# Performance work log

Hardware: AMD Instinct MI355X
Metric: run time of the kernel (lower is better)

Reference implementation:

```python
import math
import jax, jax.numpy as jnp
import numpy as np

B, T, C = 4, 2048, 1024
NH, HD = 16, 64  # n_head, head_dim
RANK = 128


def setup_inputs() -> dict:
    key = jax.random.key(0)
    ks = jax.random.split(key, 9)
    s_in = 1.0 / math.sqrt(C)
    s_r = 1.0 / math.sqrt(RANK)
    inp = {"x": jax.random.normal(ks[0], (B, T, C), dtype=jnp.float32)}
    for i, name in enumerate(["q", "k", "v", "c"]):
        inp[name + "A"] = jax.random.normal(ks[1 + 2 * i], (RANK, C), dtype=jnp.float32) * s_in
        inp[name + "B"] = jax.random.normal(ks[2 + 2 * i], (C, RANK), dtype=jnp.float32) * s_r
    return inp


def _lowrank(x, A, Bf):
    # HarmonicLinear: rank-r factorized linear, W = Bf @ A, y = x @ W^T
    return (x @ A.T) @ Bf.T


def reference(x, qA, qB, kA, kB, vA, vB, cA, cB):
    b, t, c = x.shape
    q = _lowrank(x, qA, qB).reshape(b, t, NH, HD).transpose(0, 2, 1, 3)  # [b,h,t,d]
    k = _lowrank(x, kA, kB).reshape(b, t, NH, HD).transpose(0, 2, 1, 3)
    v = _lowrank(x, vA, vB).reshape(b, t, NH, HD).transpose(0, 2, 1, 3)
    att = jnp.einsum("bhqd,bhkd->bhqk", q, k) * (1.0 / math.sqrt(HD))
    causal = jnp.tril(jnp.ones((t, t), dtype=bool))
    att = jnp.where(causal, att, -jnp.inf)
    att = jax.nn.softmax(att, axis=-1)
    y = jnp.einsum("bhqk,bhkd->bhqd", att, v)
    y = y.transpose(0, 2, 1, 3).reshape(b, t, c)
    return _lowrank(y, cA, cB)
```

## Files before the change

### kernel.cpp

```cpp
#include <hip/hip_runtime.h>

typedef unsigned short u16;
typedef __attribute__((ext_vector_type(8))) short bf16x8;
typedef __attribute__((ext_vector_type(4))) float f32x4;
typedef __attribute__((ext_vector_type(16))) float f32x16;
typedef __attribute__((ext_vector_type(4))) int i32x4;

typedef const __attribute__((address_space(1))) void gvoid_t;
typedef __attribute__((address_space(3))) void svoid_t;

__device__ __forceinline__ u16 f2bf(float f) {
  unsigned u = __builtin_bit_cast(unsigned, f);
  u += 0x7fffu + ((u >> 16) & 1u);
  return (u16)(u >> 16);
}

__device__ __forceinline__ unsigned cvtpk(float a, float b) {
  unsigned r;
  asm("v_cvt_pk_bf16_f32 %0, %1, %2" : "=v"(r) : "v"(a), "v"(b));
  return r;
}

__device__ __forceinline__ void gload_lds16(const u16* g, u16* ldsbase) {
  __builtin_amdgcn_global_load_lds((gvoid_t*)g, (svoid_t*)ldsbase, 16, 0, 0);
}

__device__ __forceinline__ void mfma16(f32x4& d, bf16x8 a, bf16x8 b) {
  asm("v_mfma_f32_16x16x32_bf16 %0, %1, %2, %0" : "+v"(d) : "v"(a), "v"(b));
}
__device__ __forceinline__ void mfma32(f32x16& d, bf16x8 a, bf16x8 b) {
  asm("v_mfma_f32_32x32x16_bf16 %0, %1, %2, %0" : "+v"(d) : "v"(a), "v"(b));
}
__device__ __forceinline__ void mfma_fence4(f32x4& a, f32x4& b, f32x4& c, f32x4& d) {
  asm volatile("s_nop 7\n\ts_nop 7" : "+v"(a), "+v"(b), "+v"(c), "+v"(d));
}
__device__ __forceinline__ void fence16x2(f32x16& a, f32x16& b) {
  asm volatile("s_nop 7\n\ts_nop 7\n\ts_nop 7" : "+v"(a), "+v"(b));
}

struct W8 { const float* s[8]; };
__global__ __launch_bounds__(256) void cvt_w_kernel(W8 w, u16* __restrict__ wb) {
  const int b = blockIdx.x;
  const int wi = b >> 7;
  const int wo = b & 127;
  const float* src = w.s[wi];
  u16* dst = wb + (size_t)wi * 131072;
  int i = (wo * 256 + (int)threadIdx.x) * 4;
  float4 v = *(const float4*)(src + i);
  ushort4 o = {f2bf(v.x), f2bf(v.y), f2bf(v.z), f2bf(v.w)};
  *(ushort4*)(dst + i) = o;
}

struct G3 { const u16* A[3]; const u16* B[3]; void* C[3]; float osc[3]; int vt[3]; };

template <typename OutT, int BM, bool CVTA, bool XCDMAP>
__global__ __launch_bounds__(256) void gemm_nt(G3 g, int M, int N, int K) {
  constexpr int NI = (BM == 128) ? 4 : 2;
  __shared__ __align__(16) u16 At[2][BM * 64];
  __shared__ __align__(16) u16 Bt[2][128 * 64];
  int bx = blockIdx.x, by = blockIdx.y, bz = blockIdx.z;
  if constexpr (XCDMAP) {
    const int xcd = bx & 7, slot = bx >> 3;
    bz = slot % 3;
    bx = xcd * 16 + slot / 3;
    by = 0;
  }
  const int z = bz;
  const u16* __restrict__ A = g.A[z];
  const float* __restrict__ Af = (const float*)g.A[z];
  const u16* __restrict__ Bw = g.B[z];
  const float osc = g.osc[z];
  const int tid = threadIdx.x;
  const int lane = tid & 63, w = tid >> 6;
  const int wm = (BM == 128) ? (w >> 1) : 0;
  const int wn = (BM == 128) ? (w & 1) : w;
  constexpr int WNW = (BM == 128) ? 64 : 32;
  const int l15 = lane & 15, l4 = lane >> 4;
  const int row0 = bx * BM, col0 = by * 128;
  const int srow = lane >> 3;
  const int schunk = ((lane & 7) ^ srow) * 8;
  const u16* Ag = A + (size_t)(row0 + w * 8 + srow) * K + schunk;
  const u16* Bg = Bw + (size_t)(col0 + w * 8 + srow) * K + schunk;
  f32x4 acc[4][NI] = {};
  float4 ax[4];
  auto STAGEB = [&](int k0, int buf) {
#pragma unroll
    for (int i = 0; i < 4; ++i)
      gload_lds16(Bg + (size_t)i * 32 * K + k0, &Bt[buf][(w * 8 + i * 32) * 64]);
  };
  auto STAGEA_G = [&](int k0, int buf) {
#pragma unroll
    for (int i = 0; i < BM / 32; ++i)
      gload_lds16(Ag + (size_t)i * 32 * K + k0, &At[buf][(w * 8 + i * 32) * 64]);
  };
  auto LOADA = [&](int k0) {
#pragma unroll
    for (int i = 0; i < BM / 32; ++i) {
      const float* src = Af + (size_t)(row0 + w * 8 + i * 32 + srow) * K + k0 + schunk;
      ax[2 * i] = *(const float4*)src;
      ax[2 * i + 1] = *(const float4*)(src + 4);
    }
  };
  auto WRITEA = [&](int buf) {
#pragma unroll
    for (int i = 0; i < BM / 32; ++i) {
      i32x4 d;
      d[0] = (int)cvtpk(ax[2 * i].x, ax[2 * i].y);
      d[1] = (int)cvtpk(ax[2 * i].z, ax[2 * i].w);
      d[2] = (int)cvtpk(ax[2 * i + 1].x, ax[2 * i + 1].y);
      d[3] = (int)cvtpk(ax[2 * i + 1].z, ax[2 * i + 1].w);
      *(i32x4*)&At[buf][(w * 8 + i * 32 + srow) * 64 + (lane & 7) * 8] = d;
    }
  };
  if constexpr (CVTA) LOADA(0); else STAGEA_G(0, 0);
  STAGEB(0, 0);
  if constexpr (CVTA) WRITEA(0);
  asm volatile("s_waitcnt vmcnt(0)" ::: "memory");
  __syncthreads();
  const int nk = K >> 6;
  for (int t = 0; t < nk; ++t) {
    const int cur = t & 1;
    if (t + 1 < nk) {
      if constexpr (CVTA) LOADA((t + 1) << 6); else STAGEA_G((t + 1) << 6, cur ^ 1);
      STAGEB((t + 1) << 6, cur ^ 1);
    }
#pragma unroll
    for (int kk = 0; kk < 64; kk += 32) {
      bf16x8 af[4], bfr[NI];
#pragma unroll
      for (int mi = 0; mi < 4; ++mi) {
        const int r = wm * 64 + mi * 16 + l15;
        af[mi] = *(const bf16x8*)&At[cur][r * 64 + ((kk + 8 * l4) ^ ((r & 7) << 3))];
      }
#pragma unroll
      for (int ni = 0; ni < NI; ++ni) {
        const int r = wn * WNW + ni * 16 + l15;
        bfr[ni] = *(const bf16x8*)&Bt[cur][r * 64 + ((kk + 8 * l4) ^ ((r & 7) << 3))];
      }
#pragma unroll
      for (int mi = 0; mi < 4; ++mi)
#pragma unroll
        for (int ni = 0; ni < NI; ++ni) mfma16(acc[mi][ni], af[mi], bfr[ni]);
    }
    if constexpr (CVTA) { if (t + 1 < nk) WRITEA(cur ^ 1); }
    asm volatile("s_waitcnt vmcnt(0)" ::: "memory");
    __syncthreads();
  }
#pragma unroll
  for (int mi = 0; mi < 4; ++mi)
    mfma_fence4(acc[mi][0], acc[mi][NI - 1], acc[mi][0], acc[mi][NI - 1]);
  if (g.vt[z]) {
    u16* VTo = (u16*)g.C[z];
    const int bbv = row0 >> 11;
#pragma unroll
    for (int mi = 0; mi < 4; ++mi) {
      const int r = row0 + wm * 64 + mi * 16 + l4 * 4;
      const int t0 = r & 2047;
#pragma unroll
      for (int ni = 0; ni < NI; ++ni) {
        const int c = col0 + wn * WNW + ni * 16 + l15;
        ushort4 ov = {f2bf(acc[mi][ni][0] * osc), f2bf(acc[mi][ni][1] * osc),
                      f2bf(acc[mi][ni][2] * osc), f2bf(acc[mi][ni][3] * osc)};
        *(ushort4*)(VTo + ((size_t)(bbv * 1024 + c)) * 2048 + t0) = ov;
      }
    }
  } else {
    OutT* __restrict__ C = (OutT*)g.C[z];
#pragma unroll
    for (int mi = 0; mi < 4; ++mi) {
      const int r = row0 + wm * 64 + mi * 16 + l4 * 4;
#pragma unroll
      for (int ni = 0; ni < NI; ++ni) {
        const int c = col0 + wn * WNW + ni * 16 + l15;
#pragma unroll
        for (int j = 0; j < 4; ++j) {
          float v = acc[mi][ni][j] * osc;
          if constexpr (sizeof(OutT) == 2)
            ((u16*)C)[(size_t)(r + j) * N + c] = f2bf(v);
          else
            ((float*)C)[(size_t)(r + j) * N + c] = v;
        }
      }
    }
  }
}

__global__ __launch_bounds__(256, 4) void attn_kernel(const u16* __restrict__ Qg,
                                                      const u16* __restrict__ Kg,
                                                      const u16* __restrict__ VTg,
                                                      u16* __restrict__ Yg) {
  __shared__ __align__(16) u16 Kt[2][64 * 64];
  __shared__ __align__(16) u16 Vt[2][64 * 64];
  const int tid = threadIdx.x;
  const int lane = tid & 63, w = tid >> 6;
  const int l31 = lane & 31, hi = lane >> 5;
  const int f = blockIdx.x;
  const int s = f >> 6;
  const int qt = (s < 4) ? 15 - 2 * s : (s < 8) ? 2 * s - 8
               : (s < 12) ? 30 - 2 * s : 2 * s - 23;
  const int bhid = f & 63;
  const int bb = bhid >> 4, h = bhid & 15;
  const size_t rb = (size_t)bb * 2048;
  const int h64 = h * 64;
  const int qb0 = qt << 7;
  const int qg = qb0 + w * 32 + l31;
  const int qend = qb0 + w * 32 + 31;
  const u16* Kbh = Kg + rb * 1024 + h64;
  const u16* VTbh = VTg + (size_t)bhid * 64 * 2048;
  const int srow = lane >> 3;
  const int schunk = ((lane & 7) ^ srow) * 8;

  bf16x8 qf[4];
#pragma unroll
  for (int kd = 0; kd < 4; ++kd)
    qf[kd] = *(const bf16x8*)(Qg + (rb + qg) * 1024 + h64 + kd * 16 + 8 * hi);

  f32x16 o0 = {}, o1 = {};
  const float MNEG = -30000.f;
  float lrun = 0.f;

  auto STAGE = [&](int it, int buf) {
    const int kv0 = it << 6;
    const int r0 = w * 16;
#pragma unroll
    for (int i = 0; i < 2; ++i) {
      gload_lds16(Kbh + (size_t)(kv0 + r0 + i * 8 + srow) * 1024 + schunk,
                  &Kt[buf][(r0 + i * 8) * 64]);
      gload_lds16(VTbh + (size_t)(r0 + i * 8 + srow) * 2048 + kv0 + schunk,
                  &Vt[buf][(r0 + i * 8) * 64]);
    }
  };
  STAGE(0, 0);
  asm volatile("s_waitcnt vmcnt(0)" ::: "memory");
  __syncthreads();

  const int nkv = 2 * qt + 2;
  for (int t = 0; t < nkv; ++t) {
    const int cur = t & 1;
    if (t + 1 < nkv) STAGE(t + 1, cur ^ 1);
    const int kv0 = t << 6;
    if (kv0 <= qend) {
      f32x16 s0 = {}, s1 = {};
      __builtin_amdgcn_s_setprio(1);
#pragma unroll
      for (int kd = 0; kd < 4; ++kd) {
        const int col = (kd * 16 + 8 * hi) ^ ((l31 & 7) << 3);
        bf16x8 kf0 = *(const bf16x8*)&Kt[cur][l31 * 64 + col];
        bf16x8 kf1 = *(const bf16x8*)&Kt[cur][(32 + l31) * 64 + col];
        mfma32(s0, kf0, qf[kd]);
        mfma32(s1, kf1, qf[kd]);
      }
      __builtin_amdgcn_s_setprio(0);
      fence16x2(s0, s1);
      if (kv0 + 63 > qb0 + w * 32) {
        const int lim = qg - (kv0 + 4 * hi);
#pragma unroll
        for (int r = 0; r < 16; ++r) {
          const int C0 = (r & 3) + 8 * (r >> 2);
          if (C0 > lim) s0[r] = MNEG;
          if (C0 + 32 > lim) s1[r] = MNEG;
        }
      }
#pragma unroll
      for (int r = 0; r < 16; ++r) {
        s0[r] = __builtin_amdgcn_exp2f(s0[r]);
        s1[r] = __builtin_amdgcn_exp2f(s1[r]);
      }
      float t8[8];
#pragma unroll
      for (int r = 0; r < 8; ++r)
        t8[r] = (s0[2 * r] + s0[2 * r + 1]) + (s1[2 * r] + s1[2 * r + 1]);
      float rs = ((t8[0] + t8[1]) + (t8[2] + t8[3])) +
                 ((t8[4] + t8[5]) + (t8[6] + t8[7]));
      lrun += rs + __shfl_xor(rs, 32, 64);
      i32x4 paw[4];
#pragma unroll
      for (int tl = 0; tl < 2; ++tl) {
        const f32x16& p = tl ? s1 : s0;
#pragma unroll
        for (int ks = 0; ks < 2; ++ks) {
          unsigned pk0 = cvtpk(p[8 * ks + 0], p[8 * ks + 1]);
          unsigned pk1 = cvtpk(p[8 * ks + 2], p[8 * ks + 3]);
          unsigned pk2 = cvtpk(p[8 * ks + 4], p[8 * ks + 5]);
          unsigned pk3 = cvtpk(p[8 * ks + 6], p[8 * ks + 7]);
          asm("v_permlane32_swap_b32 %0, %1" : "+v"(pk0), "+v"(pk2));
          asm("v_permlane32_swap_b32 %0, %1" : "+v"(pk1), "+v"(pk3));
          i32x4 A;
          A[0] = (int)pk0;
          A[1] = (int)pk1;
          A[2] = (int)pk2;
          A[3] = (int)pk3;
          paw[tl * 2 + ks] = A;
        }
      }
      asm volatile("s_nop 1");
      __builtin_amdgcn_s_setprio(1);
#pragma unroll
      for (int tl = 0; tl < 2; ++tl)
#pragma unroll
        for (int ks = 0; ks < 2; ++ks) {
          bf16x8 pa = __builtin_bit_cast(bf16x8, paw[tl * 2 + ks]);
          const int kvc = tl * 32 + ks * 16 + 8 * hi;
#pragma unroll
          for (int dt = 0; dt < 2; ++dt) {
            const int row = dt * 32 + l31;
            bf16x8 vf = *(const bf16x8*)&Vt[cur][row * 64 + (kvc ^ ((l31 & 7) << 3))];
            if (dt == 0) mfma32(o0, vf, pa);
            else         mfma32(o1, vf, pa);
          }
        }
      __builtin_amdgcn_s_setprio(0);
    }
    asm volatile("s_waitcnt vmcnt(0)" ::: "memory");
    __syncthreads();
  }
  fence16x2(o0, o1);
  const float inv = 1.f / lrun;
  u16* Yrow = Yg + (rb + qg) * 1024 + h64;
#pragma unroll
  for (int r = 0; r < 16; r += 2) {
    const int dbase = (r & 3) + 8 * (r >> 2) + 4 * hi;
    *(unsigned*)(Yrow + dbase) = cvtpk(o0[r] * inv, o0[r + 1] * inv);
    *(unsigned*)(Yrow + 32 + dbase) = cvtpk(o1[r] * inv, o1[r + 1] * inv);
  }
}

extern "C" void kernel_launch(void* const* d_in, const int* in_sizes, int n_in,
                              void* d_out, int out_size, void* d_ws, size_t ws_size,
                              hipStream_t stream) {
  const float* x = (const float*)d_in[0];
  char* ws = (char*)d_ws;
  u16* xb = (u16*)ws;
  u16* wb = (u16*)(ws + (16u << 20));
  u16* Rq = (u16*)(ws + (18u << 20));
  u16* Rk = (u16*)(ws + (20u << 20));
  u16* Rv = (u16*)(ws + (22u << 20));
  u16* Ry = (u16*)(ws + (24u << 20));
  u16* Qb = (u16*)(ws + (26u << 20));
  u16* Kb = (u16*)(ws + (42u << 20));
  u16* VT = (u16*)(ws + (58u << 20));
  const int WSZ = 131072;
  const float SC = 0.18033688011112042f;

  W8 wp;
  for (int i = 0; i < 8; ++i) wp.s[i] = (const float*)d_in[1 + i];
  cvt_w_kernel<<<1024, 256, 0, stream>>>(wp, wb);

  G3 g1;
  g1.A[0] = g1.A[1] = g1.A[2] = (const u16*)x;
  g1.B[0] = wb; g1.B[1] = wb + 2 * WSZ; g1.B[2] = wb + 4 * WSZ;
  g1.C[0] = Rq; g1.C[1] = Rk; g1.C[2] = Rv;
  g1.osc[0] = g1.osc[1] = g1.osc[2] = 1.f;
  g1.vt[0] = g1.vt[1] = g1.vt[2] = 0;
  gemm_nt<u16, 64, true, true><<<dim3(384), 256, 0, stream>>>(g1, 8192, 128, 1024);

  G3 g2;
  g2.A[0] = Rq; g2.A[1] = Rk; g2.A[2] = Rv;
  g2.B[0] = wb + 1 * WSZ; g2.B[1] = wb + 3 * WSZ; g2.B[2] = wb + 5 * WSZ;
  g2.C[0] = Qb; g2.C[1] = Kb; g2.C[2] = VT;
  g2.osc[0] = SC; g2.osc[1] = 1.f; g2.osc[2] = 1.f;
  g2.vt[0] = 0; g2.vt[1] = 0; g2.vt[2] = 1;
  gemm_nt<u16, 128, false, false><<<dim3(64, 8, 3), 256, 0, stream>>>(g2, 8192, 1024, 128);

  attn_kernel<<<dim3(1024), 256, 0, stream>>>(Qb, Kb, VT, xb);

  G3 g3;
  g3.A[0] = g3.A[1] = g3.A[2] = xb;
  g3.B[0] = g3.B[1] = g3.B[2] = wb + 6 * WSZ;
  g3.C[0] = g3.C[1] = g3.C[2] = Ry;
  g3.osc[0] = g3.osc[1] = g3.osc[2] = 1.f;
  g3.vt[0] = g3.vt[1] = g3.vt[2] = 0;
  gemm_nt<u16, 64, false, false><<<dim3(128, 1, 1), 256, 0, stream>>>(g3, 8192, 128, 1024);
  G3 g4;
  g4.A[0] = g4.A[1] = g4.A[2] = Ry;
  g4.B[0] = g4.B[1] = g4.B[2] = wb + 7 * WSZ;
  g4.C[0] = g4.C[1] = g4.C[2] = d_out;
  g4.osc[0] = g4.osc[1] = g4.osc[2] = 1.f;
  g4.vt[0] = g4.vt[1] = g4.vt[2] = 0;
  gemm_nt<float, 128, false, false><<<dim3(64, 8, 1), 256, 0, stream>>>(g4, 8192, 1024, 128);
}
```

Baseline: 122.9 us.

## Split-K the rank-reduction GEMMs and shrink tiles for more parallelism

The first low-rank projection GEMM now uses 32-row tiles, launching twice as many blocks. The output projection's first GEMM is split along K into two halves, each writing fp32 partials. The second GEMM sums those partials while converting to bf16 and uses 64-row tiles. The aim is to fill more CUs on the narrow N=128 GEMMs, which launched too few blocks. In exchange it adds fp32 partial traffic, an extra read, and smaller tiles with less reuse.

```diff
diff --git a/kernel.cpp b/kernel.cpp
--- a/kernel.cpp
+++ b/kernel.cpp
@@ -31,8 +31,8 @@
 __device__ __forceinline__ void mfma32(f32x16& d, bf16x8 a, bf16x8 b) {
   asm("v_mfma_f32_32x32x16_bf16 %0, %1, %2, %0" : "+v"(d) : "v"(a), "v"(b));
 }
-__device__ __forceinline__ void mfma_fence4(f32x4& a, f32x4& b, f32x4& c, f32x4& d) {
-  asm volatile("s_nop 7\n\ts_nop 7" : "+v"(a), "+v"(b), "+v"(c), "+v"(d));
+__device__ __forceinline__ void mfma_fence2(f32x4& a, f32x4& b) {
+  asm volatile("s_nop 7\n\ts_nop 7" : "+v"(a), "+v"(b));
 }
 __device__ __forceinline__ void fence16x2(f32x16& a, f32x16& b) {
   asm volatile("s_nop 7\n\ts_nop 7\n\ts_nop 7" : "+v"(a), "+v"(b));
@@ -51,25 +51,32 @@
   *(ushort4*)(dst + i) = o;
 }
 
-struct G3 { const u16* A[3]; const u16* B[3]; void* C[3]; float osc[3]; int vt[3]; };
-
-template <typename OutT, int BM, bool CVTA, bool XCDMAP>
+struct G3 {
+  const u16* A[3]; const float* A2[3]; const u16* B[3]; void* C[3];
+  float osc[3]; int vt[3]; int koff[3]; int klen;
+};
+
+template <typename OutT, int BM, int CVTMODE, bool XCDMAP>
 __global__ __launch_bounds__(256) void gemm_nt(G3 g, int M, int N, int K) {
+  constexpr int MI = (BM == 32) ? 2 : 4;
   constexpr int NI = (BM == 128) ? 4 : 2;
   __shared__ __align__(16) u16 At[2][BM * 64];
   __shared__ __align__(16) u16 Bt[2][128 * 64];
   int bx = blockIdx.x, by = blockIdx.y, bz = blockIdx.z;
   if constexpr (XCDMAP) {
+    const int rpx = (M / BM) >> 3;
     const int xcd = bx & 7, slot = bx >> 3;
     bz = slot % 3;
-    bx = xcd * 16 + slot / 3;
+    bx = xcd * rpx + slot / 3;
     by = 0;
   }
   const int z = bz;
   const u16* __restrict__ A = g.A[z];
   const float* __restrict__ Af = (const float*)g.A[z];
+  const float* __restrict__ Af2 = g.A2[z];
   const u16* __restrict__ Bw = g.B[z];
   const float osc = g.osc[z];
+  const int koff = g.koff[z];
   const int tid = threadIdx.x;
   const int lane = tid & 63, w = tid >> 6;
   const int wm = (BM == 128) ? (w >> 1) : 0;
@@ -81,8 +88,8 @@
   const int schunk = ((lane & 7) ^ srow) * 8;
   const u16* Ag = A + (size_t)(row0 + w * 8 + srow) * K + schunk;
   const u16* Bg = Bw + (size_t)(col0 + w * 8 + srow) * K + schunk;
-  f32x4 acc[4][NI] = {};
-  float4 ax[4];
+  f32x4 acc[MI][NI] = {};
+  float4 ax[2 * (BM / 32)], ax2[CVTMODE == 2 ? 2 * (BM / 32) : 1];
   auto STAGEB = [&](int k0, int buf) {
 #pragma unroll
     for (int i = 0; i < 4; ++i)
@@ -96,39 +103,50 @@
   auto LOADA = [&](int k0) {
 #pragma unroll
     for (int i = 0; i < BM / 32; ++i) {
-      const float* src = Af + (size_t)(row0 + w * 8 + i * 32 + srow) * K + k0 + schunk;
-      ax[2 * i] = *(const float4*)src;
-      ax[2 * i + 1] = *(const float4*)(src + 4);
+      const size_t off = (size_t)(row0 + w * 8 + i * 32 + srow) * K + k0 + schunk;
+      ax[2 * i] = *(const float4*)(Af + off);
+      ax[2 * i + 1] = *(const float4*)(Af + off + 4);
+      if constexpr (CVTMODE == 2) {
+        ax2[2 * i] = *(const float4*)(Af2 + off);
+        ax2[2 * i + 1] = *(const float4*)(Af2 + off + 4);
+      }
     }
   };
   auto WRITEA = [&](int buf) {
 #pragma unroll
     for (int i = 0; i < BM / 32; ++i) {
+      float4 a0 = ax[2 * i], a1 = ax[2 * i + 1];
+      if constexpr (CVTMODE == 2) {
+        const float4 b0 = ax2[2 * i], b1 = ax2[2 * i + 1];
+        a0.x += b0.x; a0.y += b0.y; a0.z += b0.z; a0.w += b0.w;
+        a1.x += b1.x; a1.y += b1.y; a1.z += b1.z; a1.w += b1.w;
+      }
       i32x4 d;
-      d[0] = (int)cvtpk(ax[2 * i].x, ax[2 * i].y);
-      d[1] = (int)cvtpk(ax[2 * i].z, ax[2 * i].w);
-      d[2] = (int)cvtpk(ax[2 * i + 1].x, ax[2 * i + 1].y);
-      d[3] = (int)cvtpk(ax[2 * i + 1].z, ax[2 * i + 1].w);
+      d[0] = (int)cvtpk(a0.x, a0.y);
+      d[1] = (int)cvtpk(a0.z, a0.w);
+      d[2] = (int)cvtpk(a1.x, a1.y);
+      d[3] = (int)cvtpk(a1.z, a1.w);
       *(i32x4*)&At[buf][(w * 8 + i * 32 + srow) * 64 + (lane & 7) * 8] = d;
     }
   };
-  if constexpr (CVTA) LOADA(0); else STAGEA_G(0, 0);
-  STAGEB(0, 0);
-  if constexpr (CVTA) WRITEA(0);
+  if constexpr (CVTMODE) LOADA(koff); else STAGEA_G(koff, 0);
+  STAGEB(koff, 0);
+  if constexpr (CVTMODE) WRITEA(0);
   asm volatile("s_waitcnt vmcnt(0)" ::: "memory");
   __syncthreads();
-  const int nk = K >> 6;
+  const int nk = g.klen >> 6;
   for (int t = 0; t < nk; ++t) {
     const int cur = t & 1;
     if (t + 1 < nk) {
-      if constexpr (CVTA) LOADA((t + 1) << 6); else STAGEA_G((t + 1) << 6, cur ^ 1);
-      STAGEB((t + 1) << 6, cur ^ 1);
+      const int k1 = koff + ((t + 1) << 6);
+      if constexpr (CVTMODE) LOADA(k1); else STAGEA_G(k1, cur ^ 1);
+      STAGEB(k1, cur ^ 1);
     }
 #pragma unroll
     for (int kk = 0; kk < 64; kk += 32) {
-      bf16x8 af[4], bfr[NI];
-#pragma unroll
-      for (int mi = 0; mi < 4; ++mi) {
+      bf16x8 af[MI], bfr[NI];
+#pragma unroll
+      for (int mi = 0; mi < MI; ++mi) {
         const int r = wm * 64 + mi * 16 + l15;
         af[mi] = *(const bf16x8*)&At[cur][r * 64 + ((kk + 8 * l4) ^ ((r & 7) << 3))];
       }
@@ -138,22 +156,21 @@
         bfr[ni] = *(const bf16x8*)&Bt[cur][r * 64 + ((kk + 8 * l4) ^ ((r & 7) << 3))];
       }
 #pragma unroll
-      for (int mi = 0; mi < 4; ++mi)
+      for (int mi = 0; mi < MI; ++mi)
 #pragma unroll
         for (int ni = 0; ni < NI; ++ni) mfma16(acc[mi][ni], af[mi], bfr[ni]);
     }
-    if constexpr (CVTA) { if (t + 1 < nk) WRITEA(cur ^ 1); }
+    if constexpr (CVTMODE != 0) { if (t + 1 < nk) WRITEA(cur ^ 1); }
     asm volatile("s_waitcnt vmcnt(0)" ::: "memory");
     __syncthreads();
   }
 #pragma unroll
-  for (int mi = 0; mi < 4; ++mi)
-    mfma_fence4(acc[mi][0], acc[mi][NI - 1], acc[mi][0], acc[mi][NI - 1]);
+  for (int mi = 0; mi < MI; ++mi) mfma_fence2(acc[mi][0], acc[mi][NI - 1]);
   if (g.vt[z]) {
     u16* VTo = (u16*)g.C[z];
     const int bbv = row0 >> 11;
 #pragma unroll
-    for (int mi = 0; mi < 4; ++mi) {
+    for (int mi = 0; mi < MI; ++mi) {
       const int r = row0 + wm * 64 + mi * 16 + l4 * 4;
       const int t0 = r & 2047;
 #pragma unroll
@@ -167,7 +184,7 @@
   } else {
     OutT* __restrict__ C = (OutT*)g.C[z];
 #pragma unroll
-    for (int mi = 0; mi < 4; ++mi) {
+    for (int mi = 0; mi < MI; ++mi) {
       const int r = row0 + wm * 64 + mi * 16 + l4 * 4;
 #pragma unroll
       for (int ni = 0; ni < NI; ++ni) {
@@ -335,10 +352,11 @@
   u16* Rq = (u16*)(ws + (18u << 20));
   u16* Rk = (u16*)(ws + (20u << 20));
   u16* Rv = (u16*)(ws + (22u << 20));
-  u16* Ry = (u16*)(ws + (24u << 20));
   u16* Qb = (u16*)(ws + (26u << 20));
   u16* Kb = (u16*)(ws + (42u << 20));
   u16* VT = (u16*)(ws + (58u << 20));
+  float* Ry0 = (float*)(ws + (18u << 20));
+  float* Ry1 = (float*)(ws + (22u << 20));
   const int WSZ = 131072;
   const float SC = 0.18033688011112042f;
 
@@ -346,36 +364,39 @@
   for (int i = 0; i < 8; ++i) wp.s[i] = (const float*)d_in[1 + i];
   cvt_w_kernel<<<1024, 256, 0, stream>>>(wp, wb);
 
-  G3 g1;
+  G3 g1 = {};
   g1.A[0] = g1.A[1] = g1.A[2] = (const u16*)x;
   g1.B[0] = wb; g1.B[1] = wb + 2 * WSZ; g1.B[2] = wb + 4 * WSZ;
   g1.C[0] = Rq; g1.C[1] = Rk; g1.C[2] = Rv;
   g1.osc[0] = g1.osc[1] = g1.osc[2] = 1.f;
-  g1.vt[0] = g1.vt[1] = g1.vt[2] = 0;
-  gemm_nt<u16, 64, true, true><<<dim3(384), 256, 0, stream>>>(g1, 8192, 128, 1024);
-
-  G3 g2;
+  g1.klen = 1024;
+  gemm_nt<u16, 32, 1, true><<<dim3(768), 256, 0, stream>>>(g1, 8192, 128, 1024);
+
+  G3 g2 = {};
   g2.A[0] = Rq; g2.A[1] = Rk; g2.A[2] = Rv;
   g2.B[0] = wb + 1 * WSZ; g2.B[1] = wb + 3 * WSZ; g2.B[2] = wb + 5 * WSZ;
   g2.C[0] = Qb; g2.C[1] = Kb; g2.C[2] = VT;
   g2.osc[0] = SC; g2.osc[1] = 1.f; g2.osc[2] = 1.f;
-  g2.vt[0] = 0; g2.vt[1] = 0; g2.vt[2] = 1;
-  gemm_nt<u16, 128, false, false><<<dim3(64, 8, 3), 256, 0, stream>>>(g2, 8192, 1024, 128);
+  g2.vt[2] = 1;
+  g2.klen = 128;
+  gemm_nt<u16, 128, 0, false><<<dim3(64, 8, 3), 256, 0, stream>>>(g2, 8192, 1024, 128);
 
   attn_kernel<<<dim3(1024), 256, 0, stream>>>(Qb, Kb, VT, xb);
 
-  G3 g3;
-  g3.A[0] = g3.A[1] = g3.A[2] = xb;
-  g3.B[0] = g3.B[1] = g3.B[2] = wb + 6 * WSZ;
-  g3.C[0] = g3.C[1] = g3.C[2] = Ry;
-  g3.osc[0] = g3.osc[1] = g3.osc[2] = 1.f;
-  g3.vt[0] = g3.vt[1] = g3.vt[2] = 0;
-  gemm_nt<u16, 64, false, false><<<dim3(128, 1, 1), 256, 0, stream>>>(g3, 8192, 128, 1024);
-  G3 g4;
-  g4.A[0] = g4.A[1] = g4.A[2] = Ry;
-  g4.B[0] = g4.B[1] = g4.B[2] = wb + 7 * WSZ;
-  g4.C[0] = g4.C[1] = g4.C[2] = d_out;
-  g4.osc[0] = g4.osc[1] = g4.osc[2] = 1.f;
-  g4.vt[0] = g4.vt[1] = g4.vt[2] = 0;
-  gemm_nt<float, 128, false, false><<<dim3(64, 8, 1), 256, 0, stream>>>(g4, 8192, 1024, 128);
-}
+  G3 g3 = {};
+  g3.A[0] = g3.A[1] = xb;
+  g3.B[0] = g3.B[1] = wb + 6 * WSZ;
+  g3.C[0] = Ry0; g3.C[1] = Ry1;
+  g3.osc[0] = g3.osc[1] = 1.f;
+  g3.koff[0] = 0; g3.koff[1] = 512;
+  g3.klen = 512;
+  gemm_nt<float, 32, 0, false><<<dim3(256, 1, 2), 256, 0, stream>>>(g3, 8192, 128, 1024);
+
+  G3 g4 = {};
+  g4.A[0] = (const u16*)Ry0; g4.A2[0] = Ry1;
+  g4.B[0] = wb + 7 * WSZ;
+  g4.C[0] = d_out;
+  g4.osc[0] = 1.f;
+  g4.klen = 128;
+  gemm_nt<float, 64, 2, false><<<dim3(128, 8, 1), 256, 0, stream>>>(g4, 8192, 1024, 128);
+}
```

Measured after the change: 120.6 us (median of 2 runs). About the same (-1.9%).
